# Performance work log

Hardware: AMD Instinct MI355X
Metric: run time of the kernel (lower is better)

The kernel has to match this reference:

```python
import jax, jax.numpy as jnp
import numpy as np

B, C, H, W = 4, 256, 32, 32
NUM_HEADS = 8
DK = C // NUM_HEADS


def _conv1x1(x_bcn, Wt, b):
    # x_bcn: [B, C, N]; Wt: [C_out, C_in]; b: [C_out]
    return jnp.einsum('oc,bcn->bon', Wt, x_bcn) + b[None, :, None]


def setup_inputs() -> dict:
    key = jax.random.key(0)
    ks = jax.random.split(key, 12)
    shp = (B, C, H, W)
    s = 1.0 / np.sqrt(C)
    return {
        'x0': jax.random.normal(ks[0], shp, jnp.float32),
        'x1': jax.random.normal(ks[1], shp, jnp.float32),
        'x2': jax.random.normal(ks[2], shp, jnp.float32),
        'gamma': jnp.ones((1,), jnp.float32),
        'gamma_1': jnp.ones((1,), jnp.float32),
        'gamma_2': jnp.ones((1,), jnp.float32),
        'Wq': jax.random.normal(ks[3], (C, C), jnp.float32) * s,
        'bq': jnp.zeros((C,), jnp.float32),
        'Wk': jax.random.normal(ks[4], (C, C), jnp.float32) * s,
        'bk': jnp.zeros((C,), jnp.float32),
        'Wv': jax.random.normal(ks[5], (C, C), jnp.float32) * s,
        'bv': jnp.zeros((C,), jnp.float32),
        'Wo': jax.random.normal(ks[6], (C, C), jnp.float32) * s,
        'bo': jnp.zeros((C,), jnp.float32),
    }


def reference(x0, x1, x2, gamma, gamma_1, gamma_2, Wq, bq, Wk, bk, Wv, bv, Wo, bo):
    h, dk = NUM_HEADS, DK
    N = H * W
    s0 = gamma * x0
    s1 = gamma_1 * x1
    s2 = gamma_2 * x2
    s0f = s0.reshape(B, C, N)
    streams = jnp.stack([s0f, s1.reshape(B, C, N), s2.reshape(B, C, N)], axis=1)  # [B,3,C,N]
    # Q: [B, h, N, dk]
    Q = _conv1x1(s0f, Wq, bq).reshape(B, h, dk, N).transpose(0, 1, 3, 2)
    kv_in = streams.reshape(B * 3, C, N)
    # K, V: [B, 3, h, dk, N] -> [B, h, 3N, dk]
    K = _conv1x1(kv_in, Wk, bk).reshape(B, 3, h, dk, N).transpose(0, 2, 1, 4, 3).reshape(B, h, 3 * N, dk)
    V = _conv1x1(kv_in, Wv, bv).reshape(B, 3, h, dk, N).transpose(0, 2, 1, 4, 3).reshape(B, h, 3 * N, dk)
    scores = jnp.einsum('bhqd,bhkd->bhqk', Q, K) / jnp.sqrt(jnp.float32(dk))  # [B,h,N,3N]
    attn = jax.nn.softmax(scores, axis=-1)
    out = jnp.einsum('bhqk,bhkd->bhqd', attn, V)  # [B,h,N,dk]
    out = out.transpose(0, 1, 3, 2).reshape(B, C, N)  # [B,C,N]
    fused = _conv1x1(out, Wo, bo).reshape(B, C, H, W)
    return fused
```

## Files before the change

### kernel.cpp

```cpp
#include <hip/hip_runtime.h>

typedef short bf16x8 __attribute__((ext_vector_type(8)));
typedef float f32x4  __attribute__((ext_vector_type(4)));
typedef short sh4    __attribute__((ext_vector_type(4)));
typedef float fl4    __attribute__((ext_vector_type(4)));
typedef unsigned u32x2 __attribute__((ext_vector_type(2)));
typedef unsigned u32x4 __attribute__((ext_vector_type(4)));

#define B_N  4
#define C_N  256
#define NH_N 8
#define DK_N 32
#define N_N  1024
#define KN_N 3072

#if defined(__has_builtin)
#if __has_builtin(__builtin_amdgcn_permlane32_swap) && __has_builtin(__builtin_amdgcn_permlane16_swap)
#define USE_PERMLANE 1
#endif
#endif
#ifndef USE_PERMLANE
#define USE_PERMLANE 0
#endif

__device__ __forceinline__ short f2bf(float f) {
    union { float f; unsigned u; } v; v.f = f;
    unsigned r = v.u + 0x7fffu + ((v.u >> 16) & 1u);
    return (short)(r >> 16);
}
__device__ __forceinline__ unsigned fbits(float f) {
    union { float f; unsigned u; } v; v.f = f; return v.u;
}

__global__ __launch_bounds__(256) void wcvt_kernel(
    const float* __restrict__ Wq, const float* __restrict__ Wk,
    const float* __restrict__ Wv, const float* __restrict__ Wo,
    short* __restrict__ dst) {
    int t = blockIdx.x * 256 + threadIdx.x;
    int e = t * 4;
    int m = e >> 16;
    int off = e & 65535;
    const float* src = (m == 0) ? Wq : (m == 1) ? Wk : (m == 2) ? Wv : Wo;
    fl4 v = *reinterpret_cast<const fl4*>(src + off);
    sh4 o;
    o.x = f2bf(v.x); o.y = f2bf(v.y); o.z = f2bf(v.z); o.w = f2bf(v.w);
    *reinterpret_cast<sh4*>(dst + m * 65536 + off) = o;
}

__global__ __launch_bounds__(256) void qkv_kernel(
    const short* __restrict__ Wbf, const float* __restrict__ bq,
    const float* __restrict__ bk, const float* __restrict__ bv,
    const float* __restrict__ x0, const float* __restrict__ x1,
    const float* __restrict__ x2, const float* __restrict__ g0,
    const float* __restrict__ g1, const float* __restrict__ g2,
    short* __restrict__ Qs, short* __restrict__ Ks, short* __restrict__ Vt) {
    __shared__ char smem[16640];
    __shared__ short Bt[64][264];
    float (*stage)[65] = reinterpret_cast<float(*)[65]>(smem);
    short* SM = reinterpret_cast<short*>(smem);

    int b = blockIdx.z, mt = blockIdx.y, ct = blockIdx.x;
    int lane = threadIdx.x & 63, w = threadIdx.x >> 6;
    int l16 = lane & 15, quad = lane >> 4;
    int m0 = mt * 64;

    int type, s, n0;
    if (ct < 16)      { type = 0; s = 0;                 n0 = ct * 64; }
    else if (ct < 64) { type = 1; int c2 = ct - 16; s = c2 >> 4; n0 = (c2 & 15) * 64; }
    else              { type = 2; int c2 = ct - 64; s = c2 >> 4; n0 = (c2 & 15) * 64; }

    const float* xs = (s == 0) ? x0 : (s == 1) ? x1 : x2;
    float g = (s == 0) ? g0[0] : (s == 1) ? g1[0] : g2[0];
    int tx = threadIdx.x & 63, ty = threadIdx.x >> 6;
#pragma unroll
    for (int cb = 0; cb < 4; ++cb) {
        int c0 = cb * 64;
        const float* src = xs + ((size_t)(b * C_N + c0)) * N_N + n0;
#pragma unroll
        for (int r = 0; r < 16; ++r) {
            int cl = ty * 16 + r;
            stage[cl][tx] = src[cl * N_N + tx] * g;
        }
        __syncthreads();
#pragma unroll
        for (int r = 0; r < 16; ++r) {
            int nl = ty * 16 + r;
            Bt[nl][c0 + tx] = f2bf(stage[tx][nl]);
        }
        __syncthreads();
    }

    f32x4 acc[4];
#pragma unroll
    for (int i = 0; i < 4; ++i) acc[i] = f32x4{0.f, 0.f, 0.f, 0.f};

    if (type < 2) {
        const short* A    = Wbf + type * 65536;
        const float* bias = (type == 0) ? bq : bk;
        int arow = m0 + w * 16 + l16;
#pragma unroll
        for (int kc = 0; kc < 256; kc += 32) {
            bf16x8 a = *reinterpret_cast<const bf16x8*>(A + arow * C_N + kc + quad * 8);
#pragma unroll
            for (int nt = 0; nt < 4; ++nt) {
                bf16x8 bb = *reinterpret_cast<const bf16x8*>(&Bt[nt * 16 + l16][kc + quad * 8]);
                acc[nt] = __builtin_amdgcn_mfma_f32_16x16x32_bf16(a, bb, acc[nt], 0, 0, 0);
            }
        }
        const float QSCALE = 0.17677669529663687f * 1.4426950408889634f;
        int row0 = m0 + w * 16 + quad * 4;
        float b0_ = bias[row0], b1_ = bias[row0 + 1], b2_ = bias[row0 + 2], b3_ = bias[row0 + 3];
        int dk0 = (w & 1) * 16 + quad * 4;
        short* Tp = SM + (w >> 1) * 2560 + dk0;
#pragma unroll
        for (int nt = 0; nt < 4; ++nt) {
            int pos = nt * 16 + l16;
            float v0 = acc[nt][0] + b0_, v1 = acc[nt][1] + b1_;
            float v2 = acc[nt][2] + b2_, v3 = acc[nt][3] + b3_;
            sh4 pk;
            if (type == 0) {
                pk.x = f2bf(v0 * QSCALE); pk.y = f2bf(v1 * QSCALE);
                pk.z = f2bf(v2 * QSCALE); pk.w = f2bf(v3 * QSCALE);
            } else {
                pk.x = f2bf(v0); pk.y = f2bf(v1); pk.z = f2bf(v2); pk.w = f2bf(v3);
            }
            *reinterpret_cast<sh4*>(Tp + pos * 40) = pk;
        }
        __syncthreads();
        int t = threadIdx.x;
        int pos_l = t >> 2, seg = t & 3;
#pragma unroll
        for (int hl = 0; hl < 2; ++hl) {
            bf16x8 vv = *reinterpret_cast<const bf16x8*>(SM + hl * 2560 + pos_l * 40 + seg * 8);
            int h = 2 * mt + hl;
            if (type == 0) {
                size_t base = ((size_t)(b * NH_N + h) * N_N + n0) * DK_N;
                *reinterpret_cast<bf16x8*>(Qs + base + t * 8) = vv;
            } else {
                size_t base = ((size_t)(b * NH_N + h) * KN_N + s * N_N + n0) * DK_N;
                *reinterpret_cast<bf16x8*>(Ks + base + t * 8) = vv;
            }
        }
    } else {
        const short* Bw = Wbf + 2 * 65536;
#pragma unroll
        for (int kc = 0; kc < 256; kc += 32) {
            bf16x8 ax = *reinterpret_cast<const bf16x8*>(&Bt[w * 16 + l16][kc + quad * 8]);
#pragma unroll
            for (int c2 = 0; c2 < 4; ++c2) {
                bf16x8 bw = *reinterpret_cast<const bf16x8*>(Bw + (size_t)(m0 + c2 * 16 + l16) * C_N + kc + quad * 8);
                acc[c2] = __builtin_amdgcn_mfma_f32_16x16x32_bf16(ax, bw, acc[c2], 0, 0, 0);
            }
        }
        int key0 = w * 16 + quad * 4;
#pragma unroll
        for (int c2 = 0; c2 < 4; ++c2) {
            int row = c2 * 16 + l16;
            float bb_ = bv[m0 + row];
            sh4 pk;
            pk.x = f2bf(acc[c2][0] + bb_); pk.y = f2bf(acc[c2][1] + bb_);
            pk.z = f2bf(acc[c2][2] + bb_); pk.w = f2bf(acc[c2][3] + bb_);
            *reinterpret_cast<sh4*>(SM + row * 72 + key0) = pk;
        }
        __syncthreads();
        int t = threadIdx.x;
#pragma unroll
        for (int i = 0; i < 2; ++i) {
            int ch = t + i * 256;
            int row = ch >> 3, seg = ch & 7;
            bf16x8 vv = *reinterpret_cast<const bf16x8*>(SM + row * 72 + seg * 8);
            int co = m0 + row;
            int h = co >> 5, d = co & 31;
            *reinterpret_cast<bf16x8*>(
                Vt + ((size_t)(b * NH_N + h) * DK_N + d) * KN_N + s * N_N + n0 + seg * 8) = vv;
        }
    }
}

struct Frags { bf16x8 k0, k1, k2, k3, v00, v01, v10, v11; };

__device__ __forceinline__ Frags ldfr(const short* Kp, const short* Vp0, int k0) {
    Frags f;
    f.k0  = *reinterpret_cast<const bf16x8*>(Kp + (k0 +  0) * DK_N);
    f.k1  = *reinterpret_cast<const bf16x8*>(Kp + (k0 + 16) * DK_N);
    f.k2  = *reinterpret_cast<const bf16x8*>(Kp + (k0 + 32) * DK_N);
    f.k3  = *reinterpret_cast<const bf16x8*>(Kp + (k0 + 48) * DK_N);
    f.v00 = *reinterpret_cast<const bf16x8*>(Vp0 + k0);
    f.v01 = *reinterpret_cast<const bf16x8*>(Vp0 + 16 * KN_N + k0);
    f.v10 = *reinterpret_cast<const bf16x8*>(Vp0 + k0 + 32);
    f.v11 = *reinterpret_cast<const bf16x8*>(Vp0 + 16 * KN_N + k0 + 32);
    return f;
}

#define EXPPACK(sv, Ra, Rb, LACC) {                             \
    float p0 = __builtin_amdgcn_exp2f(sv[0]);                   \
    float p1 = __builtin_amdgcn_exp2f(sv[1]);                   \
    float p2 = __builtin_amdgcn_exp2f(sv[2]);                   \
    float p3 = __builtin_amdgcn_exp2f(sv[3]);                   \
    LACC += (p0 + p1) + (p2 + p3);                              \
    Ra = __builtin_amdgcn_perm(fbits(p1), fbits(p0), 0x07060302u); \
    Rb = __builtin_amdgcn_perm(fbits(p3), fbits(p2), 0x07060302u); \
}

#if USE_PERMLANE
#define PVSTEP(RA0, RA1, RB0, RB1, VF0, VF1, O0, O1) {                 \
    unsigned x0 = RA0, y0 = RB0, x1 = RA1, y1 = RB1;                   \
    u32x2 r_;                                                          \
    r_ = __builtin_amdgcn_permlane32_swap(x0, y0, false, false); x0 = r_.x; y0 = r_.y; \
    r_ = __builtin_amdgcn_permlane16_swap(x0, y0, false, false); x0 = r_.x; y0 = r_.y; \
    r_ = __builtin_amdgcn_permlane32_swap(x1, y1, false, false); x1 = r_.x; y1 = r_.y; \
    r_ = __builtin_amdgcn_permlane16_swap(x1, y1, false, false); x1 = r_.x; y1 = r_.y; \
    union { u32x4 u; bf16x8 b; } pf_; pf_.u = u32x4{x0, x1, y0, y1};   \
    O0 = __builtin_amdgcn_mfma_f32_16x16x32_bf16(VF0, pf_.b, O0, 0, 0, 0); \
    O1 = __builtin_amdgcn_mfma_f32_16x16x32_bf16(VF1, pf_.b, O1, 0, 0, 0); \
}
#else
#define PVSTEP(RA0, RA1, RB0, RB1, VF0, VF1, O0, O1) {                 \
    union { u32x2 u; sh4 s; } wa_, wb_;                                \
    wa_.u = u32x2{RA0, RA1}; wb_.u = u32x2{RB0, RB1};                  \
    *reinterpret_cast<sh4*>(&PT[w][l16][quad * 4])      = wa_.s;       \
    *reinterpret_cast<sh4*>(&PT[w][l16][16 + quad * 4]) = wb_.s;       \
    bf16x8 pf_ = *reinterpret_cast<bf16x8*>(&PT[w][l16][quad * 8]);    \
    O0 = __builtin_amdgcn_mfma_f32_16x16x32_bf16(VF0, pf_, O0, 0, 0, 0); \
    O1 = __builtin_amdgcn_mfma_f32_16x16x32_bf16(VF1, pf_, O1, 0, 0, 0); \
}
#endif

#define PROCJ(f, QF, LACC, O0, O1) {                                     \
    f32x4 s0 = __builtin_amdgcn_mfma_f32_16x16x32_bf16(f.k0, QF, zero, 0, 0, 0); \
    f32x4 s1 = __builtin_amdgcn_mfma_f32_16x16x32_bf16(f.k1, QF, zero, 0, 0, 0); \
    f32x4 s2 = __builtin_amdgcn_mfma_f32_16x16x32_bf16(f.k2, QF, zero, 0, 0, 0); \
    f32x4 s3 = __builtin_amdgcn_mfma_f32_16x16x32_bf16(f.k3, QF, zero, 0, 0, 0); \
    unsigned R00, R01, R10, R11, R20, R21, R30, R31;                     \
    EXPPACK(s0, R00, R01, LACC); EXPPACK(s1, R10, R11, LACC);            \
    EXPPACK(s2, R20, R21, LACC); EXPPACK(s3, R30, R31, LACC);            \
    PVSTEP(R00, R01, R10, R11, f.v00, f.v01, O0, O1);                    \
    PVSTEP(R20, R21, R30, R31, f.v10, f.v11, O0, O1);                    \
}

#define PROCALL(f) {                                                     \
    PROCJ(f, qf0, la0, o00, o01);                                        \
    PROCJ(f, qf1, la1, o10, o11);                                        \
    PROCJ(f, qf2, la2, o20, o21);                                        \
    PROCJ(f, qf3, la3, o30, o31);                                        \
}

__global__ __launch_bounds__(256, 2) void attn_kernel(
    const short* __restrict__ Qs, const short* __restrict__ Ks,
    const short* __restrict__ Vt, short* __restrict__ Ot) {
    __shared__ float OL[4][64][36];
    __shared__ float Ll[4][64];
#if !USE_PERMLANE
    __shared__ short PT[4][16][36];
#endif

    int bh = blockIdx.x;
    int q0 = blockIdx.y * 64;
    int t = threadIdx.x, lane = t & 63, w = t >> 6;
    int l16 = lane & 15, quad = lane >> 4;

    const short* Qbase = Qs + ((size_t)bh * N_N + q0 + l16) * DK_N + quad * 8;
    bf16x8 qf0 = *reinterpret_cast<const bf16x8*>(Qbase + 0 * 16 * DK_N);
    bf16x8 qf1 = *reinterpret_cast<const bf16x8*>(Qbase + 1 * 16 * DK_N);
    bf16x8 qf2 = *reinterpret_cast<const bf16x8*>(Qbase + 2 * 16 * DK_N);
    bf16x8 qf3 = *reinterpret_cast<const bf16x8*>(Qbase + 3 * 16 * DK_N);
    const short* Kp  = Ks + ((size_t)bh * KN_N + l16) * DK_N + quad * 8;
    const short* Vp0 = Vt + ((size_t)bh * DK_N + l16) * KN_N + quad * 8;

    const f32x4 zero = {0.f, 0.f, 0.f, 0.f};
    f32x4 o00 = zero, o01 = zero, o10 = zero, o11 = zero;
    f32x4 o20 = zero, o21 = zero, o30 = zero, o31 = zero;
    float la0 = 0.f, la1 = 0.f, la2 = 0.f, la3 = 0.f;
    int kbase = w * 768;

    Frags cur = ldfr(Kp, Vp0, kbase);
#pragma unroll 2
    for (int i = 0; i < 11; ++i) {
        Frags nxt = ldfr(Kp, Vp0, kbase + (i + 1) * 64);
        PROCALL(cur);
        cur = nxt;
    }
    PROCALL(cur);

    la0 += __shfl_xor(la0, 16); la0 += __shfl_xor(la0, 32);
    la1 += __shfl_xor(la1, 16); la1 += __shfl_xor(la1, 32);
    la2 += __shfl_xor(la2, 16); la2 += __shfl_xor(la2, 32);
    la3 += __shfl_xor(la3, 16); la3 += __shfl_xor(la3, 32);

    *reinterpret_cast<fl4*>(&OL[w][ 0 + l16][quad * 4])      = o00;
    *reinterpret_cast<fl4*>(&OL[w][ 0 + l16][16 + quad * 4]) = o01;
    *reinterpret_cast<fl4*>(&OL[w][16 + l16][quad * 4])      = o10;
    *reinterpret_cast<fl4*>(&OL[w][16 + l16][16 + quad * 4]) = o11;
    *reinterpret_cast<fl4*>(&OL[w][32 + l16][quad * 4])      = o20;
    *reinterpret_cast<fl4*>(&OL[w][32 + l16][16 + quad * 4]) = o21;
    *reinterpret_cast<fl4*>(&OL[w][48 + l16][quad * 4])      = o30;
    *reinterpret_cast<fl4*>(&OL[w][48 + l16][16 + quad * 4]) = o31;
    if (quad == 0) {
        Ll[w][ 0 + l16] = la0;
        Ll[w][16 + l16] = la1;
        Ll[w][32 + l16] = la2;
        Ll[w][48 + l16] = la3;
    }
    __syncthreads();

    int q = t >> 2, d0 = (t & 3) * 8;
    float rl = 1.0f / (Ll[0][q] + Ll[1][q] + Ll[2][q] + Ll[3][q]);
    fl4 a0 = *reinterpret_cast<fl4*>(&OL[0][q][d0]);
    fl4 a1 = *reinterpret_cast<fl4*>(&OL[0][q][d0 + 4]);
#pragma unroll
    for (int s = 1; s < 4; ++s) {
        fl4 b0 = *reinterpret_cast<fl4*>(&OL[s][q][d0]);
        fl4 b1 = *reinterpret_cast<fl4*>(&OL[s][q][d0 + 4]);
        a0.x += b0.x; a0.y += b0.y; a0.z += b0.z; a0.w += b0.w;
        a1.x += b1.x; a1.y += b1.y; a1.z += b1.z; a1.w += b1.w;
    }
    union { sh4 s[2]; bf16x8 v; } pk;
    pk.s[0].x = f2bf(a0.x * rl); pk.s[0].y = f2bf(a0.y * rl);
    pk.s[0].z = f2bf(a0.z * rl); pk.s[0].w = f2bf(a0.w * rl);
    pk.s[1].x = f2bf(a1.x * rl); pk.s[1].y = f2bf(a1.y * rl);
    pk.s[1].z = f2bf(a1.z * rl); pk.s[1].w = f2bf(a1.w * rl);
    int b = bh >> 3, h = bh & 7;
    *reinterpret_cast<bf16x8*>(
        Ot + ((size_t)b * N_N + q0 + q) * C_N + h * DK_N + d0) = pk.v;
}

__global__ __launch_bounds__(256) void oproj_kernel(
    const short* __restrict__ Wo_bf, const float* __restrict__ bo,
    const short* __restrict__ Ot, float* __restrict__ out) {
    int b = blockIdx.z, mt = blockIdx.y, ct = blockIdx.x;
    int lane = threadIdx.x & 63, w = threadIdx.x >> 6;
    int l16 = lane & 15, quad = lane >> 4;
    int m0 = mt * 64, n0 = ct * 32;
    const short* Bsrc = Ot + ((size_t)b * N_N + n0) * C_N;
    int arow = m0 + w * 16 + l16;

    f32x4 acc[2];
    acc[0] = f32x4{0.f, 0.f, 0.f, 0.f};
    acc[1] = f32x4{0.f, 0.f, 0.f, 0.f};

#pragma unroll
    for (int kc = 0; kc < 256; kc += 32) {
        bf16x8 a = *reinterpret_cast<const bf16x8*>(Wo_bf + arow * C_N + kc + quad * 8);
#pragma unroll
        for (int nt = 0; nt < 2; ++nt) {
            bf16x8 bb = *reinterpret_cast<const bf16x8*>(Bsrc + (nt * 16 + l16) * C_N + kc + quad * 8);
            acc[nt] = __builtin_amdgcn_mfma_f32_16x16x32_bf16(a, bb, acc[nt], 0, 0, 0);
        }
    }

#pragma unroll
    for (int r = 0; r < 4; ++r) {
        int row = m0 + w * 16 + quad * 4 + r;
        float bias = bo[row];
#pragma unroll
        for (int nt = 0; nt < 2; ++nt) {
            out[((size_t)b * C_N + row) * N_N + n0 + nt * 16 + l16] = acc[nt][r] + bias;
        }
    }
}

extern "C" void kernel_launch(void* const* d_in, const int* in_sizes, int n_in,
                              void* d_out, int out_size, void* d_ws, size_t ws_size,
                              hipStream_t stream) {
    const float* x0 = (const float*)d_in[0];
    const float* x1 = (const float*)d_in[1];
    const float* x2 = (const float*)d_in[2];
    const float* g0 = (const float*)d_in[3];
    const float* g1 = (const float*)d_in[4];
    const float* g2 = (const float*)d_in[5];
    const float* Wq = (const float*)d_in[6];
    const float* bq = (const float*)d_in[7];
    const float* Wk = (const float*)d_in[8];
    const float* bk = (const float*)d_in[9];
    const float* Wv = (const float*)d_in[10];
    const float* bv = (const float*)d_in[11];
    const float* Wo = (const float*)d_in[12];
    const float* bo = (const float*)d_in[13];
    float* out = (float*)d_out;

    char* wsb = (char*)d_ws;
    short* Wbf = (short*)(wsb + 0);
    short* Qs  = (short*)(wsb + 6815744);
    short* Ks  = (short*)(wsb + 8912896);
    short* Vt  = (short*)(wsb + 15204352);
    short* Ot  = (short*)(wsb + 21495808);

    wcvt_kernel<<<256, 256, 0, stream>>>(Wq, Wk, Wv, Wo, Wbf);
    qkv_kernel<<<dim3(112, 4, 4), 256, 0, stream>>>(Wbf, bq, bk, bv,
                                                    x0, x1, x2, g0, g1, g2,
                                                    Qs, Ks, Vt);
    attn_kernel<<<dim3(32, 16), 256, 0, stream>>>(Qs, Ks, Vt, Ot);
    oproj_kernel<<<dim3(32, 4, 4), 256, 0, stream>>>(Wbf + 3 * 65536, bo, Ot, out);
}
```

Baseline: 148.0 us.

## Pretranspose activations once and fuse Q/K/V projections per tile

Input streams are now scaled, converted to bf16 and transposed once in a prep kernel (merged with the weight conversion) into a swizzled Xt buffer. The QKV kernel loads that tile straight into LDS via global_load_lds and computes K, V (and Q for stream 0) from the same tile, where before each projection type re-read and re-transposed the fp32 inputs. This removes redundant input reads and transposes and cuts the QKV grid from 112 to 48 column tiles. The attention kernel also gains s_setprio hints around its MFMA groups. The cost is an extra intermediate buffer round trip and higher register use from three accumulator sets.

```diff
diff --git a/kernel.cpp b/kernel.cpp
--- a/kernel.cpp
+++ b/kernel.cpp
@@ -32,147 +32,197 @@
     union { float f; unsigned u; } v; v.f = f; return v.u;
 }
 
-__global__ __launch_bounds__(256) void wcvt_kernel(
+__device__ __forceinline__ int stg_idx(int c, int n) {
+    return c * 64 + ((((n >> 2) ^ (c >> 2)) & 15) << 2) + (n & 3);
+}
+
+__global__ __launch_bounds__(256) void prep_kernel(
+    const float* __restrict__ x0, const float* __restrict__ x1,
+    const float* __restrict__ x2, const float* __restrict__ g0,
+    const float* __restrict__ g1, const float* __restrict__ g2,
     const float* __restrict__ Wq, const float* __restrict__ Wk,
     const float* __restrict__ Wv, const float* __restrict__ Wo,
-    short* __restrict__ dst) {
-    int t = blockIdx.x * 256 + threadIdx.x;
-    int e = t * 4;
-    int m = e >> 16;
-    int off = e & 65535;
-    const float* src = (m == 0) ? Wq : (m == 1) ? Wk : (m == 2) ? Wv : Wo;
-    fl4 v = *reinterpret_cast<const fl4*>(src + off);
-    sh4 o;
-    o.x = f2bf(v.x); o.y = f2bf(v.y); o.z = f2bf(v.z); o.w = f2bf(v.w);
-    *reinterpret_cast<sh4*>(dst + m * 65536 + off) = o;
+    short* __restrict__ Xt, short* __restrict__ Wbf) {
+    __shared__ float stage[4096];
+    int bx = blockIdx.x, t = threadIdx.x;
+    if (bx >= 192) {
+        int e = (bx - 192) * 4096 + t * 16;
+        int m = e >> 16, off = e & 65535;
+        const float* src = (m == 0) ? Wq : (m == 1) ? Wk : (m == 2) ? Wv : Wo;
+        short* dst = Wbf + m * 65536 + off;
+#pragma unroll
+        for (int j = 0; j < 4; ++j) {
+            fl4 v = *reinterpret_cast<const fl4*>(src + off + j * 4);
+            sh4 o;
+            o.x = f2bf(v.x); o.y = f2bf(v.y); o.z = f2bf(v.z); o.w = f2bf(v.w);
+            *reinterpret_cast<sh4*>(dst + j * 4) = o;
+        }
+        return;
+    }
+    int bs = bx >> 4;
+    int n0 = (bx & 15) << 6;
+    int b = bs / 3, s = bs - b * 3;
+    const float* xs = (s == 0) ? x0 : (s == 1) ? x1 : x2;
+    float g = (s == 0) ? g0[0] : (s == 1) ? g1[0] : g2[0];
+    const float* srcb = xs + (size_t)b * C_N * N_N;
+    int n4 = (t & 15) << 2;
+    for (int ch = 0; ch < 4; ++ch) {
+        int c0 = ch << 6;
+#pragma unroll
+        for (int r = 0; r < 4; ++r) {
+            int cl = (t >> 4) + (r << 4);
+            fl4 v = *reinterpret_cast<const fl4*>(srcb + (size_t)(c0 + cl) * N_N + n0 + n4);
+            v.x *= g; v.y *= g; v.z *= g; v.w *= g;
+            *reinterpret_cast<fl4*>(&stage[stg_idx(cl, n4)]) = v;
+        }
+        __syncthreads();
+#pragma unroll
+        for (int j = 0; j < 2; ++j) {
+            int u = t + (j << 8);
+            int nl = u >> 3, cg = (u & 7) << 3;
+            union { bf16x8 v8; short s16[8]; } pk;
+#pragma unroll
+            for (int i = 0; i < 8; ++i) pk.s16[i] = f2bf(stage[stg_idx(cg + i, nl)]);
+            size_t rowsh = ((size_t)bs * N_N + n0 + nl) * C_N;
+            unsigned cb = ((unsigned)((c0 + cg) * 2)) ^ ((unsigned)((nl & 7) << 4));
+            *reinterpret_cast<bf16x8*>((char*)Xt + rowsh * 2 + cb) = pk.v8;
+        }
+        __syncthreads();
+    }
 }
 
 __global__ __launch_bounds__(256) void qkv_kernel(
     const short* __restrict__ Wbf, const float* __restrict__ bq,
     const float* __restrict__ bk, const float* __restrict__ bv,
-    const float* __restrict__ x0, const float* __restrict__ x1,
-    const float* __restrict__ x2, const float* __restrict__ g0,
-    const float* __restrict__ g1, const float* __restrict__ g2,
+    const short* __restrict__ Xt,
     short* __restrict__ Qs, short* __restrict__ Ks, short* __restrict__ Vt) {
-    __shared__ char smem[16640];
-    __shared__ short Bt[64][264];
-    float (*stage)[65] = reinterpret_cast<float(*)[65]>(smem);
-    short* SM = reinterpret_cast<short*>(smem);
-
+    __shared__ short Bt[16384];
     int b = blockIdx.z, mt = blockIdx.y, ct = blockIdx.x;
-    int lane = threadIdx.x & 63, w = threadIdx.x >> 6;
+    int s = ct >> 4, n0 = (ct & 15) << 6;
+    int t = threadIdx.x, lane = t & 63, w = t >> 6;
     int l16 = lane & 15, quad = lane >> 4;
-    int m0 = mt * 64;
-
-    int type, s, n0;
-    if (ct < 16)      { type = 0; s = 0;                 n0 = ct * 64; }
-    else if (ct < 64) { type = 1; int c2 = ct - 16; s = c2 >> 4; n0 = (c2 & 15) * 64; }
-    else              { type = 2; int c2 = ct - 64; s = c2 >> 4; n0 = (c2 & 15) * 64; }
-
-    const float* xs = (s == 0) ? x0 : (s == 1) ? x1 : x2;
-    float g = (s == 0) ? g0[0] : (s == 1) ? g1[0] : g2[0];
-    int tx = threadIdx.x & 63, ty = threadIdx.x >> 6;
-#pragma unroll
-    for (int cb = 0; cb < 4; ++cb) {
-        int c0 = cb * 64;
-        const float* src = xs + ((size_t)(b * C_N + c0)) * N_N + n0;
-#pragma unroll
-        for (int r = 0; r < 16; ++r) {
-            int cl = ty * 16 + r;
-            stage[cl][tx] = src[cl * N_N + tx] * g;
-        }
-        __syncthreads();
-#pragma unroll
-        for (int r = 0; r < 16; ++r) {
-            int nl = ty * 16 + r;
-            Bt[nl][c0 + tx] = f2bf(stage[tx][nl]);
-        }
-        __syncthreads();
-    }
-
-    f32x4 acc[4];
-#pragma unroll
-    for (int i = 0; i < 4; ++i) acc[i] = f32x4{0.f, 0.f, 0.f, 0.f};
-
-    if (type < 2) {
-        const short* A    = Wbf + type * 65536;
-        const float* bias = (type == 0) ? bq : bk;
-        int arow = m0 + w * 16 + l16;
-#pragma unroll
-        for (int kc = 0; kc < 256; kc += 32) {
-            bf16x8 a = *reinterpret_cast<const bf16x8*>(A + arow * C_N + kc + quad * 8);
-#pragma unroll
-            for (int nt = 0; nt < 4; ++nt) {
-                bf16x8 bb = *reinterpret_cast<const bf16x8*>(&Bt[nt * 16 + l16][kc + quad * 8]);
-                acc[nt] = __builtin_amdgcn_mfma_f32_16x16x32_bf16(a, bb, acc[nt], 0, 0, 0);
+    int m0 = mt << 6;
+    bool hasQ = (s == 0);
+
+    const char* gsrc = (const char*)(Xt + (((size_t)(b * 3 + s)) * N_N + n0) * C_N);
+    char* ldst = (char*)Bt;
+#pragma unroll
+    for (int i = 0; i < 8; ++i) {
+        int off = ((w << 3) + i) << 10;
+        __builtin_amdgcn_global_load_lds(
+            (const __attribute__((address_space(1))) void*)(gsrc + off + lane * 16),
+            (__attribute__((address_space(3))) void*)(ldst + off), 16, 0, 0);
+    }
+    __syncthreads();
+
+    f32x4 aq[4], ak[4], av[4];
+#pragma unroll
+    for (int i = 0; i < 4; ++i) {
+        aq[i] = f32x4{0.f, 0.f, 0.f, 0.f};
+        ak[i] = f32x4{0.f, 0.f, 0.f, 0.f};
+        av[i] = f32x4{0.f, 0.f, 0.f, 0.f};
+    }
+    const short* WqA = Wbf;
+    const short* WkA = Wbf + 65536;
+    const short* WvA = Wbf + 131072;
+    int arow = m0 + (w << 4) + l16;
+    unsigned xv = (unsigned)((l16 & 7) << 4);
+    const char* btb = (const char*)Bt;
+#pragma unroll
+    for (int kc = 0; kc < 256; kc += 32) {
+        unsigned colb = ((unsigned)((kc + quad * 8) * 2)) ^ xv;
+        bf16x8 bt0 = *reinterpret_cast<const bf16x8*>(btb + ((0  + l16) << 9) + colb);
+        bf16x8 bt1 = *reinterpret_cast<const bf16x8*>(btb + ((16 + l16) << 9) + colb);
+        bf16x8 bt2 = *reinterpret_cast<const bf16x8*>(btb + ((32 + l16) << 9) + colb);
+        bf16x8 bt3 = *reinterpret_cast<const bf16x8*>(btb + ((48 + l16) << 9) + colb);
+        bf16x8 wk = *reinterpret_cast<const bf16x8*>(WkA + (size_t)arow * C_N + kc + quad * 8);
+        ak[0] = __builtin_amdgcn_mfma_f32_16x16x32_bf16(wk, bt0, ak[0], 0, 0, 0);
+        ak[1] = __builtin_amdgcn_mfma_f32_16x16x32_bf16(wk, bt1, ak[1], 0, 0, 0);
+        ak[2] = __builtin_amdgcn_mfma_f32_16x16x32_bf16(wk, bt2, ak[2], 0, 0, 0);
+        ak[3] = __builtin_amdgcn_mfma_f32_16x16x32_bf16(wk, bt3, ak[3], 0, 0, 0);
+        bf16x8 wv = *reinterpret_cast<const bf16x8*>(WvA + (size_t)arow * C_N + kc + quad * 8);
+        av[0] = __builtin_amdgcn_mfma_f32_16x16x32_bf16(wv, bt0, av[0], 0, 0, 0);
+        av[1] = __builtin_amdgcn_mfma_f32_16x16x32_bf16(wv, bt1, av[1], 0, 0, 0);
+        av[2] = __builtin_amdgcn_mfma_f32_16x16x32_bf16(wv, bt2, av[2], 0, 0, 0);
+        av[3] = __builtin_amdgcn_mfma_f32_16x16x32_bf16(wv, bt3, av[3], 0, 0, 0);
+        if (hasQ) {
+            bf16x8 wq = *reinterpret_cast<const bf16x8*>(WqA + (size_t)arow * C_N + kc + quad * 8);
+            aq[0] = __builtin_amdgcn_mfma_f32_16x16x32_bf16(wq, bt0, aq[0], 0, 0, 0);
+            aq[1] = __builtin_amdgcn_mfma_f32_16x16x32_bf16(wq, bt1, aq[1], 0, 0, 0);
+            aq[2] = __builtin_amdgcn_mfma_f32_16x16x32_bf16(wq, bt2, aq[2], 0, 0, 0);
+            aq[3] = __builtin_amdgcn_mfma_f32_16x16x32_bf16(wq, bt3, aq[3], 0, 0, 0);
+        }
+    }
+    __syncthreads();
+
+    short* SMq = Bt;
+    short* SMk = Bt + 5120;
+    short* SMv = Bt + 10240;
+    int row0 = m0 + (w << 4) + (quad << 2);
+    int dk0 = ((w & 1) << 4) + (quad << 2);
+    {
+        float kb0 = bk[row0], kb1 = bk[row0 + 1], kb2 = bk[row0 + 2], kb3 = bk[row0 + 3];
+        short* Tp = SMk + (w >> 1) * 2560 + dk0;
+#pragma unroll
+        for (int nt = 0; nt < 4; ++nt) {
+            int pos = (nt << 4) + l16;
+            sh4 pk;
+            pk.x = f2bf(ak[nt][0] + kb0); pk.y = f2bf(ak[nt][1] + kb1);
+            pk.z = f2bf(ak[nt][2] + kb2); pk.w = f2bf(ak[nt][3] + kb3);
+            *reinterpret_cast<sh4*>(Tp + pos * 40) = pk;
+        }
+    }
+    if (hasQ) {
+        const float QSCALE = 0.17677669529663687f * 1.4426950408889634f;
+        float qb0 = bq[row0], qb1 = bq[row0 + 1], qb2 = bq[row0 + 2], qb3 = bq[row0 + 3];
+        short* Tp = SMq + (w >> 1) * 2560 + dk0;
+#pragma unroll
+        for (int nt = 0; nt < 4; ++nt) {
+            int pos = (nt << 4) + l16;
+            sh4 pk;
+            pk.x = f2bf((aq[nt][0] + qb0) * QSCALE); pk.y = f2bf((aq[nt][1] + qb1) * QSCALE);
+            pk.z = f2bf((aq[nt][2] + qb2) * QSCALE); pk.w = f2bf((aq[nt][3] + qb3) * QSCALE);
+            *reinterpret_cast<sh4*>(Tp + pos * 40) = pk;
+        }
+    }
+    {
+        int crow = (w << 4) + (quad << 2);
+        float vb0 = bv[m0 + crow], vb1 = bv[m0 + crow + 1];
+        float vb2 = bv[m0 + crow + 2], vb3 = bv[m0 + crow + 3];
+#pragma unroll
+        for (int nt = 0; nt < 4; ++nt) {
+            int pos = (nt << 4) + l16;
+            SMv[(crow + 0) * 72 + pos] = f2bf(av[nt][0] + vb0);
+            SMv[(crow + 1) * 72 + pos] = f2bf(av[nt][1] + vb1);
+            SMv[(crow + 2) * 72 + pos] = f2bf(av[nt][2] + vb2);
+            SMv[(crow + 3) * 72 + pos] = f2bf(av[nt][3] + vb3);
+        }
+    }
+    __syncthreads();
+
+    {
+        int pos_l = t >> 2, seg = t & 3;
+#pragma unroll
+        for (int hl = 0; hl < 2; ++hl) {
+            int h = 2 * mt + hl;
+            bf16x8 kv = *reinterpret_cast<const bf16x8*>(SMk + hl * 2560 + pos_l * 40 + seg * 8);
+            *reinterpret_cast<bf16x8*>(
+                Ks + ((size_t)(b * NH_N + h) * KN_N + s * N_N + n0) * DK_N + t * 8) = kv;
+            if (hasQ) {
+                bf16x8 qv = *reinterpret_cast<const bf16x8*>(SMq + hl * 2560 + pos_l * 40 + seg * 8);
+                *reinterpret_cast<bf16x8*>(
+                    Qs + ((size_t)(b * NH_N + h) * N_N + n0) * DK_N + t * 8) = qv;
             }
         }
-        const float QSCALE = 0.17677669529663687f * 1.4426950408889634f;
-        int row0 = m0 + w * 16 + quad * 4;
-        float b0_ = bias[row0], b1_ = bias[row0 + 1], b2_ = bias[row0 + 2], b3_ = bias[row0 + 3];
-        int dk0 = (w & 1) * 16 + quad * 4;
-        short* Tp = SM + (w >> 1) * 2560 + dk0;
-#pragma unroll
-        for (int nt = 0; nt < 4; ++nt) {
-            int pos = nt * 16 + l16;
-            float v0 = acc[nt][0] + b0_, v1 = acc[nt][1] + b1_;
-            float v2 = acc[nt][2] + b2_, v3 = acc[nt][3] + b3_;
-            sh4 pk;
-            if (type == 0) {
-                pk.x = f2bf(v0 * QSCALE); pk.y = f2bf(v1 * QSCALE);
-                pk.z = f2bf(v2 * QSCALE); pk.w = f2bf(v3 * QSCALE);
-            } else {
-                pk.x = f2bf(v0); pk.y = f2bf(v1); pk.z = f2bf(v2); pk.w = f2bf(v3);
-            }
-            *reinterpret_cast<sh4*>(Tp + pos * 40) = pk;
-        }
-        __syncthreads();
-        int t = threadIdx.x;
-        int pos_l = t >> 2, seg = t & 3;
-#pragma unroll
-        for (int hl = 0; hl < 2; ++hl) {
-            bf16x8 vv = *reinterpret_cast<const bf16x8*>(SM + hl * 2560 + pos_l * 40 + seg * 8);
-            int h = 2 * mt + hl;
-            if (type == 0) {
-                size_t base = ((size_t)(b * NH_N + h) * N_N + n0) * DK_N;
-                *reinterpret_cast<bf16x8*>(Qs + base + t * 8) = vv;
-            } else {
-                size_t base = ((size_t)(b * NH_N + h) * KN_N + s * N_N + n0) * DK_N;
-                *reinterpret_cast<bf16x8*>(Ks + base + t * 8) = vv;
-            }
-        }
-    } else {
-        const short* Bw = Wbf + 2 * 65536;
-#pragma unroll
-        for (int kc = 0; kc < 256; kc += 32) {
-            bf16x8 ax = *reinterpret_cast<const bf16x8*>(&Bt[w * 16 + l16][kc + quad * 8]);
-#pragma unroll
-            for (int c2 = 0; c2 < 4; ++c2) {
-                bf16x8 bw = *reinterpret_cast<const bf16x8*>(Bw + (size_t)(m0 + c2 * 16 + l16) * C_N + kc + quad * 8);
-                acc[c2] = __builtin_amdgcn_mfma_f32_16x16x32_bf16(ax, bw, acc[c2], 0, 0, 0);
-            }
-        }
-        int key0 = w * 16 + quad * 4;
-#pragma unroll
-        for (int c2 = 0; c2 < 4; ++c2) {
-            int row = c2 * 16 + l16;
-            float bb_ = bv[m0 + row];
-            sh4 pk;
-            pk.x = f2bf(acc[c2][0] + bb_); pk.y = f2bf(acc[c2][1] + bb_);
-            pk.z = f2bf(acc[c2][2] + bb_); pk.w = f2bf(acc[c2][3] + bb_);
-            *reinterpret_cast<sh4*>(SM + row * 72 + key0) = pk;
-        }
-        __syncthreads();
-        int t = threadIdx.x;
 #pragma unroll
         for (int i = 0; i < 2; ++i) {
-            int ch = t + i * 256;
-            int row = ch >> 3, seg = ch & 7;
-            bf16x8 vv = *reinterpret_cast<const bf16x8*>(SM + row * 72 + seg * 8);
+            int chn = t + (i << 8);
+            int row = chn >> 3, seg2 = chn & 7;
+            bf16x8 vv = *reinterpret_cast<const bf16x8*>(SMv + row * 72 + seg2 * 8);
             int co = m0 + row;
             int h = co >> 5, d = co & 31;
             *reinterpret_cast<bf16x8*>(
-                Vt + ((size_t)(b * NH_N + h) * DK_N + d) * KN_N + s * N_N + n0 + seg * 8) = vv;
+                Vt + ((size_t)(b * NH_N + h) * DK_N + d) * KN_N + s * N_N + n0 + seg2 * 8) = vv;
         }
     }
 }
@@ -211,8 +261,10 @@
     r_ = __builtin_amdgcn_permlane32_swap(x1, y1, false, false); x1 = r_.x; y1 = r_.y; \
     r_ = __builtin_amdgcn_permlane16_swap(x1, y1, false, false); x1 = r_.x; y1 = r_.y; \
     union { u32x4 u; bf16x8 b; } pf_; pf_.u = u32x4{x0, x1, y0, y1};   \
+    __builtin_amdgcn_s_setprio(1);                                     \
     O0 = __builtin_amdgcn_mfma_f32_16x16x32_bf16(VF0, pf_.b, O0, 0, 0, 0); \
     O1 = __builtin_amdgcn_mfma_f32_16x16x32_bf16(VF1, pf_.b, O1, 0, 0, 0); \
+    __builtin_amdgcn_s_setprio(0);                                     \
 }
 #else
 #define PVSTEP(RA0, RA1, RB0, RB1, VF0, VF1, O0, O1) {                 \
@@ -227,10 +279,12 @@
 #endif
 
 #define PROCJ(f, QF, LACC, O0, O1) {                                     \
+    __builtin_amdgcn_s_setprio(1);                                       \
     f32x4 s0 = __builtin_amdgcn_mfma_f32_16x16x32_bf16(f.k0, QF, zero, 0, 0, 0); \
     f32x4 s1 = __builtin_amdgcn_mfma_f32_16x16x32_bf16(f.k1, QF, zero, 0, 0, 0); \
     f32x4 s2 = __builtin_amdgcn_mfma_f32_16x16x32_bf16(f.k2, QF, zero, 0, 0, 0); \
     f32x4 s3 = __builtin_amdgcn_mfma_f32_16x16x32_bf16(f.k3, QF, zero, 0, 0, 0); \
+    __builtin_amdgcn_s_setprio(0);                                       \
     unsigned R00, R01, R10, R11, R20, R21, R30, R31;                     \
     EXPPACK(s0, R00, R01, LACC); EXPPACK(s1, R10, R11, LACC);            \
     EXPPACK(s2, R20, R21, LACC); EXPPACK(s3, R30, R31, LACC);            \
@@ -380,15 +434,16 @@
 
     char* wsb = (char*)d_ws;
     short* Wbf = (short*)(wsb + 0);
+    short* Xt  = (short*)(wsb + 524288);
     short* Qs  = (short*)(wsb + 6815744);
     short* Ks  = (short*)(wsb + 8912896);
     short* Vt  = (short*)(wsb + 15204352);
     short* Ot  = (short*)(wsb + 21495808);
 
-    wcvt_kernel<<<256, 256, 0, stream>>>(Wq, Wk, Wv, Wo, Wbf);
-    qkv_kernel<<<dim3(112, 4, 4), 256, 0, stream>>>(Wbf, bq, bk, bv,
-                                                    x0, x1, x2, g0, g1, g2,
-                                                    Qs, Ks, Vt);
+    prep_kernel<<<256, 256, 0, stream>>>(x0, x1, x2, g0, g1, g2,
+                                         Wq, Wk, Wv, Wo, Xt, Wbf);
+    qkv_kernel<<<dim3(48, 4, 4), 256, 0, stream>>>(Wbf, bq, bk, bv, Xt,
+                                                   Qs, Ks, Vt);
     attn_kernel<<<dim3(32, 16), 256, 0, stream>>>(Qs, Ks, Vt, Ot);
     oproj_kernel<<<dim3(32, 4, 4), 256, 0, stream>>>(Wbf + 3 * 65536, bo, Ot, out);
 }
```

New measurement: 132.8 us. 10.3% less time.
